# Kernel optimization log

Hardware: AMD Instinct MI355X
Metric: run time of the kernel (lower is better)

## Reference

```python
import jax, jax.numpy as jnp
import numpy as np

B, N, D, H, DH = 1, 192, 128, 4, 32
INNER = H * DH  # == D


def _ln(x, g, b):
    mu = x.mean(-1, keepdims=True)
    var = ((x - mu) ** 2).mean(-1, keepdims=True)
    return (x - mu) * jax.lax.rsqrt(var + 1e-5) * g + b


def _axial(x, row, lng, lnb, wq, wkv, wo, bo, wg, bg, wb):
    # x: (B, N, N, D). row=True: attend along axis 2 (rows as batch);
    # row=False: attend along axis 1 (columns as batch).
    scale = DH ** -0.5
    # edge bias from RAW x (edges are not layer-normed in the torch code)
    bias = jnp.einsum('bijd,dh->bhij', x, wb)            # (B, H, N, N)
    xn = _ln(x, lng, lnb)
    xa = xn if row else jnp.swapaxes(xn, 1, 2)           # (B, R, S, D)
    q = (xa @ wq).reshape(B, N, N, H, DH) * scale
    kv = (xa @ wkv).reshape(B, N, N, 2, H, DH)           # chunk(2): k then v
    k, v = kv[..., 0, :, :], kv[..., 1, :, :]
    # scores: (B, R, H, q, k); same bias matrix broadcast over every row/col R
    dots = jnp.einsum('brqhe,brkhe->brhqk', q, k) + bias[:, None]
    attn = jax.nn.softmax(dots, axis=-1)
    o = jnp.einsum('brhqk,brkhe->brqhe', attn, v).reshape(B, N, N, INNER)
    gates = jax.nn.sigmoid(xa @ wg + bg)                 # sigmoid gating on pre-attn x
    out = (o * gates) @ wo + bo
    return out if row else jnp.swapaxes(out, 1, 2)


def setup_inputs() -> dict:
    key = jax.random.key(0)
    ks = iter(jax.random.split(key, 32))

    def w(shape, s=0.02):
        return jax.random.normal(next(ks), shape, dtype=jnp.float32) * s

    inp = {"x": jax.random.normal(next(ks), (B, N, N, D), dtype=jnp.float32)}
    for sfx in ("o", "i"):  # outgoing (row) / ingoing (col) triangle attention
        inp[f"lng_{sfx}"] = jnp.ones((D,), jnp.float32)
        inp[f"lnb_{sfx}"] = jnp.zeros((D,), jnp.float32)
        inp[f"wq_{sfx}"] = w((D, INNER))
        inp[f"wkv_{sfx}"] = w((D, 2 * INNER))
        inp[f"wo_{sfx}"] = w((INNER, D))
        inp[f"bo_{sfx}"] = jnp.zeros((D,), jnp.float32)
        inp[f"wg_{sfx}"] = w((D, INNER))
        inp[f"bg_{sfx}"] = jnp.ones((INNER,), jnp.float32)  # gating bias init = 1
        inp[f"wb_{sfx}"] = w((D, H))
    inp["lng_f"] = jnp.ones((D,), jnp.float32)
    inp["lnb_f"] = jnp.zeros((D,), jnp.float32)
    inp["w1"] = w((D, 8 * D))      # dim -> dim*mult*2, mult=4
    inp["b1"] = jnp.zeros((8 * D,), jnp.float32)
    inp["w2"] = w((4 * D, D))
    inp["b2"] = jnp.zeros((D,), jnp.float32)
    return inp


def reference(x, lng_o, lnb_o, wq_o, wkv_o, wo_o, bo_o, wg_o, bg_o, wb_o,
              lng_i, lnb_i, wq_i, wkv_i, wo_i, bo_i, wg_i, bg_i, wb_i,
              lng_f, lnb_f, w1, b1, w2, b2):
    x = _axial(x, True, lng_o, lnb_o, wq_o, wkv_o, wo_o, bo_o, wg_o, bg_o, wb_o) + x
    x = _axial(x, False, lng_i, lnb_i, wq_i, wkv_i, wo_i, bo_i, wg_i, bg_i, wb_i) + x
    xn = _ln(x, lng_f, lnb_f)
    h = xn @ w1 + b1
    a, g = jnp.split(h, 2, axis=-1)   # GEGLU: x * gelu(gates), exact gelu
    ff = (a * jax.nn.gelu(g, approximate=False)) @ w2 + b2
    return x + ff
```

## Files before the change

kernel.cpp:

```cpp
#include <hip/hip_runtime.h>
#include <hip/hip_bf16.h>
#include <math.h>

constexpr int NSEQ = 192;
constexpr int DIM  = 128;
constexpr int NH   = 4;
constexpr int DHEAD = 32;
constexpr int MROWS = NSEQ * NSEQ;

typedef __hip_bfloat16 bf16;
typedef __attribute__((ext_vector_type(8))) short bf16x8;
typedef __attribute__((ext_vector_type(4))) float f32x4;
typedef unsigned int u32;

__device__ __forceinline__ void gload16(const void* g, void* l) {
    __builtin_amdgcn_global_load_lds(
        (const __attribute__((address_space(1))) u32*)g,
        (__attribute__((address_space(3))) u32*)l, 16, 0, 0);
}

__device__ __forceinline__ short f2bs(float f) {
    __hip_bfloat16 h = __float2bfloat16(f);
    return *(short*)&h;
}
__device__ __forceinline__ float bs2f(unsigned short s) {
    return __uint_as_float(((u32)s) << 16);
}

__global__ __launch_bounds__(256)
void convert_weights(const float* __restrict__ wq_o, const float* __restrict__ wkv_o,
                     const float* __restrict__ wg_o,
                     const float* __restrict__ wq_i, const float* __restrict__ wkv_i,
                     const float* __restrict__ wg_i,
                     const float* __restrict__ wo_o, const float* __restrict__ wo_i,
                     const float* __restrict__ w1, const float* __restrict__ b1,
                     const float* __restrict__ w2,
                     bf16* __restrict__ WQKVG_O, bf16* __restrict__ WQKVG_I,
                     bf16* __restrict__ WOT_O, bf16* __restrict__ WOT_I,
                     bf16* __restrict__ W1PT, bf16* __restrict__ W2T,
                     float* __restrict__ B1P)
{
    int idx = blockIdx.x * 256 + threadIdx.x;
    const float scale = 0.17677669529663689f;
    if (idx < 131072) {
        int s = idx >> 16, i = idx & 65535;
        int r = i >> 7, d = i & 127;
        const float* wq  = s ? wq_i  : wq_o;
        const float* wkv = s ? wkv_i : wkv_o;
        const float* wg  = s ? wg_i  : wg_o;
        float v;
        if (r < 128)      v = wq[d * 128 + r] * scale;
        else if (r < 384) v = wkv[d * 256 + (r - 128)];
        else              v = wg[d * 128 + (r - 384)];
        (s ? WQKVG_I : WQKVG_O)[i] = __float2bfloat16(v);
    } else if (idx < 163840) {
        int i = idx - 131072; int s = i >> 14; i &= 16383;
        int r = i >> 7, d = i & 127;
        (s ? WOT_I : WOT_O)[i] = __float2bfloat16((s ? wo_i : wo_o)[d * 128 + r]);
    } else if (idx < 294912) {
        int i = idx - 163840;
        int r = i >> 7, d = i & 127;
        int col = (r & 1) ? 512 + (r >> 1) : (r >> 1);
        W1PT[i] = __float2bfloat16(w1[d * 1024 + col]);
    } else if (idx < 360448) {
        int i = idx - 294912;
        int n = i >> 9, k = i & 511;
        W2T[i] = __float2bfloat16(w2[k * 128 + n]);
    } else if (idx < 361472) {
        int r = idx - 360448;
        B1P[r] = b1[(r & 1) ? 512 + (r >> 1) : (r >> 1)];
    }
}

__global__ __launch_bounds__(256)
void ln_bias_kernel(const float* __restrict__ x, const float* __restrict__ g,
                    const float* __restrict__ b, const float* __restrict__ wb,
                    bf16* __restrict__ xa, float* __restrict__ bias, int trans)
{
    int wid  = threadIdx.x >> 6;
    int lane = threadIdx.x & 63;
    int row  = blockIdx.x * 4 + wid;
    const float* xr = x + (size_t)row * DIM;
    float x0 = xr[lane], x1 = xr[lane + 64];
    float s = x0 + x1, sq = x0 * x0 + x1 * x1;
    #pragma unroll
    for (int off = 32; off > 0; off >>= 1) {
        s  += __shfl_down(s, off);
        sq += __shfl_down(sq, off);
    }
    s = __shfl(s, 0); sq = __shfl(sq, 0);
    float mu  = s * (1.0f / 128.0f);
    float var = sq * (1.0f / 128.0f) - mu * mu;
    float rs  = rsqrtf(var + 1e-5f);
    float y0 = (x0 - mu) * rs * g[lane]      + b[lane];
    float y1 = (x1 - mu) * rs * g[lane + 64] + b[lane + 64];
    int orow = row;
    if (trans) { int i = row / NSEQ, j = row % NSEQ; orow = j * NSEQ + i; }
    bf16* yr = xa + (size_t)orow * DIM;
    yr[lane]      = __float2bfloat16(y0);
    yr[lane + 64] = __float2bfloat16(y1);
    if (wb) {
        #pragma unroll
        for (int h = 0; h < NH; ++h) {
            float bh = x0 * wb[lane * NH + h] + x1 * wb[(lane + 64) * NH + h];
            #pragma unroll
            for (int off = 32; off > 0; off >>= 1) bh += __shfl_down(bh, off);
            if (lane == 0) bias[(size_t)h * MROWS + row] = bh;
        }
    }
}

enum { EPI_QKVG = 0, EPI_OUT = 1, EPI_GEGLU = 2, EPI_FF2 = 3 };

template<int EPI, int BM, int K>
__global__ __launch_bounds__(256)
void mfma_gemm(const bf16* __restrict__ A, const bf16* __restrict__ BT,
               const float* __restrict__ e_bias,
               const float* __restrict__ e_resid,
               float* __restrict__ e_outf,
               bf16* __restrict__ e_outb,
               bf16* __restrict__ e_outb2,
               int trans)
{
    constexpr int MREP = BM / 32;
    constexpr int ABYTES = BM * 256;
    constexpr int STAGEB = ABYTES + 32768;
    constexpr int EPIB = BM * 512;
    constexpr int LDSB = STAGEB > EPIB ? STAGEB : EPIB;
    __shared__ char sm[LDSB];
    char* asb = sm;
    char* bsb = sm + ABYTES;
    float* eb = (float*)sm;

    int tid = threadIdx.x;
    int l = tid & 63, w = tid >> 6;
    int wr = w >> 1, wc = w & 1;
    int m0 = blockIdx.x * BM, n0 = blockIdx.y * 128;
    int fr = l & 15, g = l >> 4;
    int srow  = tid >> 4;
    int satom = (tid & 15) ^ (srow & 7);

    f32x4 acc[MREP][4] = {};

    for (int k0 = 0; k0 < K; k0 += 128) {
        #pragma unroll
        for (int i = 0; i < BM / 16; ++i)
            gload16(A + (size_t)(m0 + i * 16 + srow) * K + k0 + satom * 8,
                    asb + i * 4096 + w * 1024);
        #pragma unroll
        for (int i = 0; i < 8; ++i)
            gload16(BT + (size_t)(n0 + i * 16 + srow) * K + k0 + satom * 8,
                    bsb + i * 4096 + w * 1024);
        __syncthreads();
        #pragma unroll
        for (int kk = 0; kk < 4; ++kk) {
            bf16x8 af[MREP], bfr[4];
            #pragma unroll
            for (int mi = 0; mi < MREP; ++mi) {
                int r = wr * (BM / 2) + mi * 16 + fr;
                af[mi] = *(const bf16x8*)(asb + r * 256 + ((kk * 64 + g * 16) ^ ((r & 7) << 4)));
            }
            #pragma unroll
            for (int ni = 0; ni < 4; ++ni) {
                int r = wc * 64 + ni * 16 + fr;
                bfr[ni] = *(const bf16x8*)(bsb + r * 256 + ((kk * 64 + g * 16) ^ ((r & 7) << 4)));
            }
            #pragma unroll
            for (int mi = 0; mi < MREP; ++mi)
                #pragma unroll
                for (int ni = 0; ni < 4; ++ni)
                    acc[mi][ni] = __builtin_amdgcn_mfma_f32_16x16x32_bf16(
                        af[mi], bfr[ni], acc[mi][ni], 0, 0, 0);
        }
        __syncthreads();
    }

    #pragma unroll
    for (int mi = 0; mi < MREP; ++mi)
        #pragma unroll
        for (int ni = 0; ni < 4; ++ni)
            #pragma unroll
            for (int j = 0; j < 4; ++j) {
                int rl = wr * (BM / 2) + mi * 16 + g * 4 + j;
                int cl = wc * 64 + ni * 16 + fr;
                int a  = ((cl >> 2) + rl) & 31;
                eb[rl * 128 + (a << 2) + (cl & 3)] = acc[mi][ni][j];
            }
    __syncthreads();

    #pragma unroll
    for (int p = 0; p < BM / 32; ++p) {
        int c = tid + p * 256;
        int row = c >> 3;
        int ch = c & 7;
        int grow = m0 + row;
        int gc0 = ch * 16;
        float v[16];
        #pragma unroll
        for (int q = 0; q < 4; ++q) {
            f32x4 t4 = *(const f32x4*)&eb[row * 128 + (((ch * 4 + q + row) & 31) << 2)];
            v[q * 4 + 0] = t4[0]; v[q * 4 + 1] = t4[1];
            v[q * 4 + 2] = t4[2]; v[q * 4 + 3] = t4[3];
        }
        if (EPI == EPI_QKVG) {
            int seg = blockIdx.y;
            short o16[16];
            if (seg < 3) {
                #pragma unroll
                for (int i = 0; i < 16; ++i) o16[i] = f2bs(v[i]);
                int h = gc0 >> 5, e0 = gc0 & 31;
                bf16* dst = e_outb + ((size_t)(seg * NH + h) * MROWS + grow) * DHEAD + e0;
                *(uint4*)dst = *(uint4*)o16;
                *(uint4*)(dst + 8) = *(uint4*)(o16 + 8);
            } else {
                #pragma unroll
                for (int i = 0; i < 16; ++i)
                    o16[i] = f2bs(1.0f / (1.0f + __expf(-(v[i] + e_bias[gc0 + i]))));
                bf16* dst = e_outb2 + (size_t)grow * DIM + gc0;
                *(uint4*)dst = *(uint4*)o16;
                *(uint4*)(dst + 8) = *(uint4*)(o16 + 8);
            }
        } else if (EPI == EPI_OUT || EPI == EPI_FF2) {
            int orow = (EPI == EPI_OUT && trans) ? ((grow % NSEQ) * NSEQ + grow / NSEQ) : grow;
            const float* rp = e_resid + (size_t)orow * DIM + gc0;
            float* op = e_outf + (size_t)orow * DIM + gc0;
            #pragma unroll
            for (int q = 0; q < 4; ++q) {
                float4 r4 = *(const float4*)(rp + q * 4);
                float4 o4;
                o4.x = v[q*4+0] + e_bias[gc0 + q*4 + 0] + r4.x;
                o4.y = v[q*4+1] + e_bias[gc0 + q*4 + 1] + r4.y;
                o4.z = v[q*4+2] + e_bias[gc0 + q*4 + 2] + r4.z;
                o4.w = v[q*4+3] + e_bias[gc0 + q*4 + 3] + r4.w;
                *(float4*)(op + q * 4) = o4;
            }
        } else {
            short o8[8];
            #pragma unroll
            for (int t = 0; t < 8; ++t) {
                float a  = v[2*t]     + e_bias[n0 + gc0 + 2*t];
                float gg = v[2*t + 1] + e_bias[n0 + gc0 + 2*t + 1];
                float y  = 1.5957691216f * (gg + 0.044715f * gg * gg * gg);
                float ge = gg / (1.0f + __expf(-y));
                o8[t] = f2bs(a * ge);
            }
            *(uint4*)(e_outb + (size_t)grow * 512 + ((n0 + gc0) >> 1)) = *(uint4*)o8;
        }
    }
}

__global__ __launch_bounds__(256)
void attn_mfma_kernel(const bf16* __restrict__ Qh, const bf16* __restrict__ Kh,
                      const bf16* __restrict__ Vh, const float* __restrict__ BIAS,
                      const bf16* __restrict__ G, bf16* __restrict__ TMP)
{
    __shared__ unsigned short vtp[32][200];
    int h = blockIdx.x / NSEQ;
    int r = blockIdx.x % NSEQ;
    int t = threadIdx.x;
    int l = t & 63;
    int w = t >> 6;

    const bf16* vbase = Vh + ((size_t)h * MROWS + (size_t)r * NSEQ) * DHEAD;
    #pragma unroll
    for (int i = 0; i < 6; ++i) {
        int q4 = t + i * 256;
        int k = q4 >> 3, e0 = (q4 & 7) * 4;
        uint2 v = *(const uint2*)(vbase + (size_t)k * DHEAD + e0);
        int kk = k & 31, sup = k >> 5;
        int col = sup * 32 + ((kk & 15) >> 2) * 8 + (kk & 3) + ((kk >> 4) << 2);
        const unsigned short* vs = (const unsigned short*)&v;
        #pragma unroll
        for (int j = 0; j < 4; ++j) vtp[e0 + j][col] = vs[j];
    }
    __syncthreads();

    int fr = l & 15, g = l >> 4;
    int q0 = w * 48;
    const bf16*  qbase = Qh + ((size_t)h * MROWS + (size_t)r * NSEQ) * DHEAD;
    const bf16*  kbase = Kh + ((size_t)h * MROWS + (size_t)r * NSEQ) * DHEAD;
    const float* bbase = BIAS + (size_t)h * MROWS;

    bf16x8 qf[3];
    #pragma unroll
    for (int i = 0; i < 3; ++i)
        qf[i] = *(const bf16x8*)(qbase + (size_t)(q0 + i * 16 + fr) * DHEAD + g * 8);

    f32x4 ot[3][2] = {};
    float m_[3] = {-1e30f, -1e30f, -1e30f};
    float s_[3] = {};

    for (int sup = 0; sup < 6; ++sup) {
        bf16x8 kf0 = *(const bf16x8*)(kbase + (size_t)(sup * 32 + fr) * DHEAD + g * 8);
        bf16x8 kf1 = *(const bf16x8*)(kbase + (size_t)(sup * 32 + 16 + fr) * DHEAD + g * 8);
        bf16x8 pb[3];
        #pragma unroll
        for (int qt = 0; qt < 3; ++qt) {
            f32x4 z = {};
            f32x4 s0 = __builtin_amdgcn_mfma_f32_16x16x32_bf16(kf0, qf[qt], z, 0, 0, 0);
            f32x4 s1 = __builtin_amdgcn_mfma_f32_16x16x32_bf16(kf1, qf[qt], z, 0, 0, 0);
            const float* bp = bbase + (size_t)(q0 + qt * 16 + fr) * NSEQ + sup * 32 + g * 4;
            float4 b0 = *(const float4*)bp;
            float4 b1 = *(const float4*)(bp + 16);
            s0[0] += b0.x; s0[1] += b0.y; s0[2] += b0.z; s0[3] += b0.w;
            s1[0] += b1.x; s1[1] += b1.y; s1[2] += b1.z; s1[3] += b1.w;
            float tmax = fmaxf(fmaxf(fmaxf(s0[0], s0[1]), fmaxf(s0[2], s0[3])),
                               fmaxf(fmaxf(s1[0], s1[1]), fmaxf(s1[2], s1[3])));
            tmax = fmaxf(tmax, __shfl_xor(tmax, 16));
            tmax = fmaxf(tmax, __shfl_xor(tmax, 32));
            if (__any(tmax > m_[qt] + 8.0f)) {
                float mn = fmaxf(m_[qt], tmax);
                float c = __expf(m_[qt] - mn);
                s_[qt] *= c; ot[qt][0] *= c; ot[qt][1] *= c;
                m_[qt] = mn;
            }
            float p[8];
            #pragma unroll
            for (int j = 0; j < 4; ++j) p[j]     = __expf(s0[j] - m_[qt]);
            #pragma unroll
            for (int j = 0; j < 4; ++j) p[4 + j] = __expf(s1[j] - m_[qt]);
            s_[qt] += ((p[0] + p[1]) + (p[2] + p[3])) + ((p[4] + p[5]) + (p[6] + p[7]));
            bf16x8 pk;
            #pragma unroll
            for (int j = 0; j < 8; ++j) pk[j] = f2bs(p[j]);
            pb[qt] = pk;
        }
        #pragma unroll
        for (int et = 0; et < 2; ++et) {
            bf16x8 vf = *(const bf16x8*)(&vtp[et * 16 + fr][sup * 32 + g * 8]);
            #pragma unroll
            for (int qt = 0; qt < 3; ++qt)
                ot[qt][et] = __builtin_amdgcn_mfma_f32_16x16x32_bf16(vf, pb[qt], ot[qt][et], 0, 0, 0);
        }
    }

    #pragma unroll
    for (int qt = 0; qt < 3; ++qt) {
        float sq = s_[qt];
        sq += __shfl_xor(sq, 16);
        sq += __shfl_xor(sq, 32);
        float inv = 1.0f / sq;
        int q = q0 + qt * 16 + fr;
        size_t row = (size_t)r * NSEQ + q;
        #pragma unroll
        for (int et = 0; et < 2; ++et) {
            int e0 = h * DHEAD + et * 16 + g * 4;
            const bf16* gp = G + row * DIM + e0;
            u32 g01 = *(const u32*)gp;
            u32 g23 = *(const u32*)(gp + 2);
            float gx0 = __uint_as_float((g01 & 0xffffu) << 16);
            float gx1 = __uint_as_float(g01 & 0xffff0000u);
            float gx2 = __uint_as_float((g23 & 0xffffu) << 16);
            float gx3 = __uint_as_float(g23 & 0xffff0000u);
            short o4[4];
            o4[0] = f2bs(ot[qt][et][0] * inv * gx0);
            o4[1] = f2bs(ot[qt][et][1] * inv * gx1);
            o4[2] = f2bs(ot[qt][et][2] * inv * gx2);
            o4[3] = f2bs(ot[qt][et][3] * inv * gx3);
            *(uint2*)(TMP + row * DIM + e0) = *(uint2*)o4;
        }
    }
}

extern "C" void kernel_launch(void* const* d_in, const int* in_sizes, int n_in,
                              void* d_out, int out_size, void* d_ws, size_t ws_size,
                              hipStream_t stream) {
    const float* x     = (const float*)d_in[0];
    const float* lng_o = (const float*)d_in[1];
    const float* lnb_o = (const float*)d_in[2];
    const float* wq_o  = (const float*)d_in[3];
    const float* wkv_o = (const float*)d_in[4];
    const float* wo_o  = (const float*)d_in[5];
    const float* bo_o  = (const float*)d_in[6];
    const float* wg_o  = (const float*)d_in[7];
    const float* bg_o  = (const float*)d_in[8];
    const float* wb_o  = (const float*)d_in[9];
    const float* lng_i = (const float*)d_in[10];
    const float* lnb_i = (const float*)d_in[11];
    const float* wq_i  = (const float*)d_in[12];
    const float* wkv_i = (const float*)d_in[13];
    const float* wo_i  = (const float*)d_in[14];
    const float* bo_i  = (const float*)d_in[15];
    const float* wg_i  = (const float*)d_in[16];
    const float* bg_i  = (const float*)d_in[17];
    const float* wb_i  = (const float*)d_in[18];
    const float* lng_f = (const float*)d_in[19];
    const float* lnb_f = (const float*)d_in[20];
    const float* w1    = (const float*)d_in[21];
    const float* b1    = (const float*)d_in[22];
    const float* w2    = (const float*)d_in[23];
    const float* b2    = (const float*)d_in[24];

    const size_t T = (size_t)MROWS * DIM;
    char* base = (char*)d_ws;
    bf16*  XA    = (bf16*)base;  base += T * 2;
    float* X     = (float*)base; base += T * 4;
    bf16*  QKVb  = (bf16*)base;  base += 3 * T * 2;
    bf16*  Gb    = (bf16*)base;  base += T * 2;
    float* BIASb = (float*)base; base += (size_t)NH * MROWS * 4;
    bf16*  TMP   = (bf16*)base;  base += T * 2;
    bf16*  WQKVG_O = (bf16*)base; base += 512 * 128 * 2;
    bf16*  WQKVG_I = (bf16*)base; base += 512 * 128 * 2;
    bf16*  WOT_O   = (bf16*)base; base += 128 * 128 * 2;
    bf16*  WOT_I   = (bf16*)base; base += 128 * 128 * 2;
    bf16*  W1PT    = (bf16*)base; base += 1024 * 128 * 2;
    bf16*  W2T     = (bf16*)base; base += 128 * 512 * 2;
    float* B1P     = (float*)base; base += 1024 * 4;
    bf16*  H2      = (bf16*)QKVb;
    bf16*  Qhp = QKVb;
    bf16*  Khp = QKVb + T;
    bf16*  Vhp = QKVb + 2 * T;

    convert_weights<<<1412, 256, 0, stream>>>(wq_o, wkv_o, wg_o, wq_i, wkv_i, wg_i,
                                              wo_o, wo_i, w1, b1, w2,
                                              WQKVG_O, WQKVG_I, WOT_O, WOT_I,
                                              W1PT, W2T, B1P);

    dim3 gQKVG(MROWS / 128, 4), gN128(MROWS / 128, 1), gW1(MROWS / 128, 8);
    dim3 gFF2(MROWS / 64, 1);

    ln_bias_kernel<<<MROWS / 4, 256, 0, stream>>>(x, lng_o, lnb_o, wb_o, XA, BIASb, 0);
    mfma_gemm<EPI_QKVG, 128, 128><<<gQKVG, 256, 0, stream>>>(XA, WQKVG_O, bg_o, nullptr, nullptr, QKVb, Gb, 0);
    attn_mfma_kernel<<<NSEQ * NH, 256, 0, stream>>>(Qhp, Khp, Vhp, BIASb, Gb, TMP);
    mfma_gemm<EPI_OUT, 128, 128><<<gN128, 256, 0, stream>>>(TMP, WOT_O, bo_o, x, X, nullptr, nullptr, 0);

    ln_bias_kernel<<<MROWS / 4, 256, 0, stream>>>(X, lng_i, lnb_i, wb_i, XA, BIASb, 1);
    mfma_gemm<EPI_QKVG, 128, 128><<<gQKVG, 256, 0, stream>>>(XA, WQKVG_I, bg_i, nullptr, nullptr, QKVb, Gb, 0);
    attn_mfma_kernel<<<NSEQ * NH, 256, 0, stream>>>(Qhp, Khp, Vhp, BIASb, Gb, TMP);
    mfma_gemm<EPI_OUT, 128, 128><<<gN128, 256, 0, stream>>>(TMP, WOT_I, bo_i, X, X, nullptr, nullptr, 1);

    ln_bias_kernel<<<MROWS / 4, 256, 0, stream>>>(X, lng_f, lnb_f, nullptr, XA, nullptr, 0);
    mfma_gemm<EPI_GEGLU, 128, 128><<<gW1, 256, 0, stream>>>(XA, W1PT, B1P, nullptr, nullptr, H2, nullptr, 0);
    mfma_gemm<EPI_FF2, 64, 512><<<gFF2, 256, 0, stream>>>(H2, W2T, b2, X, (float*)d_out, nullptr, nullptr, 0);
}
```

Baseline: 241.0 us.

## Fuse LayerNorm and edge-bias projection into the output GEMM epilogue

The output-projection GEMM epilogue now computes the next stage's LayerNorm and the per-head edge bias from the freshly computed residual sum. It writes the normalised bf16 activations directly in the layout the next stage needs, transposed where required. This removes two standalone ln_bias kernel launches and their full re-read of the fp32 activation tensor. The GEMM also moves to a 64-wide K step with half-height epilogue staging to cut LDS usage, and declares launch bounds targeting 4 blocks per CU. The cost is more synchronisation per K loop and a heavier epilogue with cross-lane reductions.

```diff
diff --git a/kernel.cpp b/kernel.cpp
--- a/kernel.cpp
+++ b/kernel.cpp
@@ -22,9 +22,6 @@
 __device__ __forceinline__ short f2bs(float f) {
     __hip_bfloat16 h = __float2bfloat16(f);
     return *(short*)&h;
-}
-__device__ __forceinline__ float bs2f(unsigned short s) {
-    return __uint_as_float(((u32)s) << 16);
 }
 
 __global__ __launch_bounds__(256)
@@ -75,7 +72,7 @@
 __global__ __launch_bounds__(256)
 void ln_bias_kernel(const float* __restrict__ x, const float* __restrict__ g,
                     const float* __restrict__ b, const float* __restrict__ wb,
-                    bf16* __restrict__ xa, float* __restrict__ bias, int trans)
+                    bf16* __restrict__ xa, float* __restrict__ bias)
 {
     int wid  = threadIdx.x >> 6;
     int lane = threadIdx.x & 63;
@@ -94,42 +91,43 @@
     float rs  = rsqrtf(var + 1e-5f);
     float y0 = (x0 - mu) * rs * g[lane]      + b[lane];
     float y1 = (x1 - mu) * rs * g[lane + 64] + b[lane + 64];
-    int orow = row;
-    if (trans) { int i = row / NSEQ, j = row % NSEQ; orow = j * NSEQ + i; }
-    bf16* yr = xa + (size_t)orow * DIM;
+    bf16* yr = xa + (size_t)row * DIM;
     yr[lane]      = __float2bfloat16(y0);
     yr[lane + 64] = __float2bfloat16(y1);
-    if (wb) {
-        #pragma unroll
-        for (int h = 0; h < NH; ++h) {
-            float bh = x0 * wb[lane * NH + h] + x1 * wb[(lane + 64) * NH + h];
-            #pragma unroll
-            for (int off = 32; off > 0; off >>= 1) bh += __shfl_down(bh, off);
-            if (lane == 0) bias[(size_t)h * MROWS + row] = bh;
-        }
+    #pragma unroll
+    for (int h = 0; h < NH; ++h) {
+        float bh = x0 * wb[lane * NH + h] + x1 * wb[(lane + 64) * NH + h];
+        #pragma unroll
+        for (int off = 32; off > 0; off >>= 1) bh += __shfl_down(bh, off);
+        if (lane == 0) bias[(size_t)h * MROWS + row] = bh;
     }
 }
 
 enum { EPI_QKVG = 0, EPI_OUT = 1, EPI_GEGLU = 2, EPI_FF2 = 3 };
 
 template<int EPI, int BM, int K>
-__global__ __launch_bounds__(256)
+__global__ __launch_bounds__(256, 4)
 void mfma_gemm(const bf16* __restrict__ A, const bf16* __restrict__ BT,
                const float* __restrict__ e_bias,
                const float* __restrict__ e_resid,
                float* __restrict__ e_outf,
                bf16* __restrict__ e_outb,
                bf16* __restrict__ e_outb2,
+               const float* __restrict__ lng,
+               const float* __restrict__ lnb,
+               const float* __restrict__ wbp,
+               float* __restrict__ biasb,
+               bf16* __restrict__ xa,
                int trans)
 {
-    constexpr int MREP = BM / 32;
-    constexpr int ABYTES = BM * 256;
-    constexpr int STAGEB = ABYTES + 32768;
-    constexpr int EPIB = BM * 512;
-    constexpr int LDSB = STAGEB > EPIB ? STAGEB : EPIB;
+    constexpr int MREP  = BM / 32;
+    constexpr int AB    = BM * 128;
+    constexpr int STAGE = AB + 16384;
+    constexpr int EPIB  = (BM / 2) * 512;
+    constexpr int LDSB  = STAGE > EPIB ? STAGE : EPIB;
     __shared__ char sm[LDSB];
     char* asb = sm;
-    char* bsb = sm + ABYTES;
+    char* bsb = sm + AB;
     float* eb = (float*)sm;
 
     int tid = threadIdx.x;
@@ -137,33 +135,33 @@
     int wr = w >> 1, wc = w & 1;
     int m0 = blockIdx.x * BM, n0 = blockIdx.y * 128;
     int fr = l & 15, g = l >> 4;
-    int srow  = tid >> 4;
-    int satom = (tid & 15) ^ (srow & 7);
+    int lr8 = l >> 3;
+    int satom = (l & 7) ^ lr8;
 
     f32x4 acc[MREP][4] = {};
 
-    for (int k0 = 0; k0 < K; k0 += 128) {
-        #pragma unroll
-        for (int i = 0; i < BM / 16; ++i)
-            gload16(A + (size_t)(m0 + i * 16 + srow) * K + k0 + satom * 8,
+    for (int k0 = 0; k0 < K; k0 += 64) {
+        #pragma unroll
+        for (int i = 0; i < BM / 32; ++i)
+            gload16(A + (size_t)(m0 + i * 32 + w * 8 + lr8) * K + k0 + satom * 8,
                     asb + i * 4096 + w * 1024);
         #pragma unroll
-        for (int i = 0; i < 8; ++i)
-            gload16(BT + (size_t)(n0 + i * 16 + srow) * K + k0 + satom * 8,
+        for (int i = 0; i < 4; ++i)
+            gload16(BT + (size_t)(n0 + i * 32 + w * 8 + lr8) * K + k0 + satom * 8,
                     bsb + i * 4096 + w * 1024);
         __syncthreads();
         #pragma unroll
-        for (int kk = 0; kk < 4; ++kk) {
+        for (int kk = 0; kk < 2; ++kk) {
             bf16x8 af[MREP], bfr[4];
             #pragma unroll
             for (int mi = 0; mi < MREP; ++mi) {
                 int r = wr * (BM / 2) + mi * 16 + fr;
-                af[mi] = *(const bf16x8*)(asb + r * 256 + ((kk * 64 + g * 16) ^ ((r & 7) << 4)));
+                af[mi] = *(const bf16x8*)(asb + r * 128 + ((kk * 64 + g * 16) ^ ((r & 7) << 4)));
             }
             #pragma unroll
             for (int ni = 0; ni < 4; ++ni) {
                 int r = wc * 64 + ni * 16 + fr;
-                bfr[ni] = *(const bf16x8*)(bsb + r * 256 + ((kk * 64 + g * 16) ^ ((r & 7) << 4)));
+                bfr[ni] = *(const bf16x8*)(bsb + r * 128 + ((kk * 64 + g * 16) ^ ((r & 7) << 4)));
             }
             #pragma unroll
             for (int mi = 0; mi < MREP; ++mi)
@@ -176,76 +174,131 @@
     }
 
     #pragma unroll
-    for (int mi = 0; mi < MREP; ++mi)
-        #pragma unroll
-        for (int ni = 0; ni < 4; ++ni)
-            #pragma unroll
-            for (int j = 0; j < 4; ++j) {
-                int rl = wr * (BM / 2) + mi * 16 + g * 4 + j;
-                int cl = wc * 64 + ni * 16 + fr;
-                int a  = ((cl >> 2) + rl) & 31;
-                eb[rl * 128 + (a << 2) + (cl & 3)] = acc[mi][ni][j];
+    for (int rr = 0; rr < 2; ++rr) {
+        if (wr == rr) {
+            #pragma unroll
+            for (int mi = 0; mi < MREP; ++mi)
+                #pragma unroll
+                for (int ni = 0; ni < 4; ++ni)
+                    #pragma unroll
+                    for (int j = 0; j < 4; ++j) {
+                        int rl = mi * 16 + g * 4 + j;
+                        int cl = wc * 64 + ni * 16 + fr;
+                        int a  = cl >> 2;
+                        int pa = (((a >> 2) + (a & 3)) & 7) | ((a & 3) << 3);
+                        eb[rl * 128 + pa * 4 + (cl & 3)] = acc[mi][ni][j];
+                    }
+        }
+        __syncthreads();
+        #pragma unroll
+        for (int p = 0; p < BM / 64; ++p) {
+            int c = tid + p * 256;
+            int row_l = c >> 3, ch = c & 7;
+            int grow = m0 + rr * (BM / 2) + row_l;
+            int gc0 = ch * 16;
+            float v[16];
+            #pragma unroll
+            for (int q = 0; q < 4; ++q) {
+                int pa = ((ch + q) & 7) + q * 8;
+                f32x4 t4 = *(const f32x4*)&eb[row_l * 128 + pa * 4];
+                v[q * 4 + 0] = t4[0]; v[q * 4 + 1] = t4[1];
+                v[q * 4 + 2] = t4[2]; v[q * 4 + 3] = t4[3];
             }
-    __syncthreads();
-
-    #pragma unroll
-    for (int p = 0; p < BM / 32; ++p) {
-        int c = tid + p * 256;
-        int row = c >> 3;
-        int ch = c & 7;
-        int grow = m0 + row;
-        int gc0 = ch * 16;
-        float v[16];
-        #pragma unroll
-        for (int q = 0; q < 4; ++q) {
-            f32x4 t4 = *(const f32x4*)&eb[row * 128 + (((ch * 4 + q + row) & 31) << 2)];
-            v[q * 4 + 0] = t4[0]; v[q * 4 + 1] = t4[1];
-            v[q * 4 + 2] = t4[2]; v[q * 4 + 3] = t4[3];
-        }
-        if (EPI == EPI_QKVG) {
-            int seg = blockIdx.y;
-            short o16[16];
-            if (seg < 3) {
-                #pragma unroll
-                for (int i = 0; i < 16; ++i) o16[i] = f2bs(v[i]);
-                int h = gc0 >> 5, e0 = gc0 & 31;
-                bf16* dst = e_outb + ((size_t)(seg * NH + h) * MROWS + grow) * DHEAD + e0;
-                *(uint4*)dst = *(uint4*)o16;
-                *(uint4*)(dst + 8) = *(uint4*)(o16 + 8);
+            if (EPI == EPI_QKVG) {
+                int seg = blockIdx.y;
+                short o16[16];
+                if (seg < 3) {
+                    #pragma unroll
+                    for (int i = 0; i < 16; ++i) o16[i] = f2bs(v[i]);
+                    int h = ch >> 1, e0 = (ch & 1) * 16;
+                    bf16* dst = e_outb + ((size_t)(seg * NH + h) * MROWS + grow) * DHEAD + e0;
+                    *(uint4*)dst = *(uint4*)o16;
+                    *(uint4*)(dst + 8) = *(uint4*)(o16 + 8);
+                } else {
+                    #pragma unroll
+                    for (int i = 0; i < 16; ++i)
+                        o16[i] = f2bs(1.0f / (1.0f + __expf(-(v[i] + e_bias[gc0 + i]))));
+                    bf16* dst = e_outb2 + (size_t)grow * DIM + gc0;
+                    *(uint4*)dst = *(uint4*)o16;
+                    *(uint4*)(dst + 8) = *(uint4*)(o16 + 8);
+                }
+            } else if (EPI == EPI_OUT) {
+                int orow  = trans ? ((grow % NSEQ) * NSEQ + grow / NSEQ) : grow;
+                int xarow = (grow % NSEQ) * NSEQ + grow / NSEQ;
+                const float* rp = e_resid + (size_t)orow * DIM + gc0;
+                float* op = e_outf + (size_t)orow * DIM + gc0;
+                #pragma unroll
+                for (int q = 0; q < 4; ++q) {
+                    float4 r4 = *(const float4*)(rp + q * 4);
+                    v[q*4+0] += e_bias[gc0 + q*4 + 0] + r4.x;
+                    v[q*4+1] += e_bias[gc0 + q*4 + 1] + r4.y;
+                    v[q*4+2] += e_bias[gc0 + q*4 + 2] + r4.z;
+                    v[q*4+3] += e_bias[gc0 + q*4 + 3] + r4.w;
+                    *(float4*)(op + q * 4) = make_float4(v[q*4+0], v[q*4+1], v[q*4+2], v[q*4+3]);
+                }
+                float s1 = 0.f, s2 = 0.f;
+                #pragma unroll
+                for (int i = 0; i < 16; ++i) { s1 += v[i]; s2 += v[i] * v[i]; }
+                #pragma unroll
+                for (int off = 1; off < 8; off <<= 1) {
+                    s1 += __shfl_xor(s1, off);
+                    s2 += __shfl_xor(s2, off);
+                }
+                float mu  = s1 * (1.0f / 128.0f);
+                float var = s2 * (1.0f / 128.0f) - mu * mu;
+                float rs  = rsqrtf(var + 1e-5f);
+                short o16[16];
+                #pragma unroll
+                for (int i = 0; i < 16; ++i)
+                    o16[i] = f2bs((v[i] - mu) * rs * lng[gc0 + i] + lnb[gc0 + i]);
+                bf16* xd = xa + (size_t)xarow * DIM + gc0;
+                *(uint4*)xd = *(uint4*)o16;
+                *(uint4*)(xd + 8) = *(uint4*)(o16 + 8);
+                if (wbp) {
+                    float bh[NH] = {};
+                    #pragma unroll
+                    for (int i = 0; i < 16; ++i) {
+                        float vv = v[i];
+                        #pragma unroll
+                        for (int h = 0; h < NH; ++h)
+                            bh[h] = fmaf(vv, wbp[(gc0 + i) * NH + h], bh[h]);
+                    }
+                    #pragma unroll
+                    for (int off = 1; off < 8; off <<= 1)
+                        #pragma unroll
+                        for (int h = 0; h < NH; ++h) bh[h] += __shfl_xor(bh[h], off);
+                    if (ch == 0)
+                        #pragma unroll
+                        for (int h = 0; h < NH; ++h)
+                            biasb[(size_t)h * MROWS + grow] = bh[h];
+                }
+            } else if (EPI == EPI_FF2) {
+                const float* rp = e_resid + (size_t)grow * DIM + gc0;
+                float* op = e_outf + (size_t)grow * DIM + gc0;
+                #pragma unroll
+                for (int q = 0; q < 4; ++q) {
+                    float4 r4 = *(const float4*)(rp + q * 4);
+                    float4 o4;
+                    o4.x = v[q*4+0] + e_bias[gc0 + q*4 + 0] + r4.x;
+                    o4.y = v[q*4+1] + e_bias[gc0 + q*4 + 1] + r4.y;
+                    o4.z = v[q*4+2] + e_bias[gc0 + q*4 + 2] + r4.z;
+                    o4.w = v[q*4+3] + e_bias[gc0 + q*4 + 3] + r4.w;
+                    *(float4*)(op + q * 4) = o4;
+                }
             } else {
-                #pragma unroll
-                for (int i = 0; i < 16; ++i)
-                    o16[i] = f2bs(1.0f / (1.0f + __expf(-(v[i] + e_bias[gc0 + i]))));
-                bf16* dst = e_outb2 + (size_t)grow * DIM + gc0;
-                *(uint4*)dst = *(uint4*)o16;
-                *(uint4*)(dst + 8) = *(uint4*)(o16 + 8);
+                short o8[8];
+                #pragma unroll
+                for (int t = 0; t < 8; ++t) {
+                    float a  = v[2*t]     + e_bias[n0 + gc0 + 2*t];
+                    float gg = v[2*t + 1] + e_bias[n0 + gc0 + 2*t + 1];
+                    float y  = 1.5957691216f * (gg + 0.044715f * gg * gg * gg);
+                    float ge = gg / (1.0f + __expf(-y));
+                    o8[t] = f2bs(a * ge);
+                }
+                *(uint4*)(e_outb + (size_t)grow * 512 + ((n0 + gc0) >> 1)) = *(uint4*)o8;
             }
-        } else if (EPI == EPI_OUT || EPI == EPI_FF2) {
-            int orow = (EPI == EPI_OUT && trans) ? ((grow % NSEQ) * NSEQ + grow / NSEQ) : grow;
-            const float* rp = e_resid + (size_t)orow * DIM + gc0;
-            float* op = e_outf + (size_t)orow * DIM + gc0;
-            #pragma unroll
-            for (int q = 0; q < 4; ++q) {
-                float4 r4 = *(const float4*)(rp + q * 4);
-                float4 o4;
-                o4.x = v[q*4+0] + e_bias[gc0 + q*4 + 0] + r4.x;
-                o4.y = v[q*4+1] + e_bias[gc0 + q*4 + 1] + r4.y;
-                o4.z = v[q*4+2] + e_bias[gc0 + q*4 + 2] + r4.z;
-                o4.w = v[q*4+3] + e_bias[gc0 + q*4 + 3] + r4.w;
-                *(float4*)(op + q * 4) = o4;
-            }
-        } else {
-            short o8[8];
-            #pragma unroll
-            for (int t = 0; t < 8; ++t) {
-                float a  = v[2*t]     + e_bias[n0 + gc0 + 2*t];
-                float gg = v[2*t + 1] + e_bias[n0 + gc0 + 2*t + 1];
-                float y  = 1.5957691216f * (gg + 0.044715f * gg * gg * gg);
-                float ge = gg / (1.0f + __expf(-y));
-                o8[t] = f2bs(a * ge);
-            }
-            *(uint4*)(e_outb + (size_t)grow * 512 + ((n0 + gc0) >> 1)) = *(uint4*)o8;
-        }
+        }
+        __syncthreads();
     }
 }
 
@@ -416,20 +469,30 @@
                                               WQKVG_O, WQKVG_I, WOT_O, WOT_I,
                                               W1PT, W2T, B1P);
 
-    dim3 gQKVG(MROWS / 128, 4), gN128(MROWS / 128, 1), gW1(MROWS / 128, 8);
+    dim3 gQKVG(MROWS / 128, 4), gOUT(MROWS / 128, 1), gW1(MROWS / 128, 8);
     dim3 gFF2(MROWS / 64, 1);
 
-    ln_bias_kernel<<<MROWS / 4, 256, 0, stream>>>(x, lng_o, lnb_o, wb_o, XA, BIASb, 0);
-    mfma_gemm<EPI_QKVG, 128, 128><<<gQKVG, 256, 0, stream>>>(XA, WQKVG_O, bg_o, nullptr, nullptr, QKVb, Gb, 0);
+    ln_bias_kernel<<<MROWS / 4, 256, 0, stream>>>(x, lng_o, lnb_o, wb_o, XA, BIASb);
+    mfma_gemm<EPI_QKVG, 128, 128><<<gQKVG, 256, 0, stream>>>(
+        XA, WQKVG_O, bg_o, nullptr, nullptr, QKVb, Gb,
+        nullptr, nullptr, nullptr, nullptr, nullptr, 0);
     attn_mfma_kernel<<<NSEQ * NH, 256, 0, stream>>>(Qhp, Khp, Vhp, BIASb, Gb, TMP);
-    mfma_gemm<EPI_OUT, 128, 128><<<gN128, 256, 0, stream>>>(TMP, WOT_O, bo_o, x, X, nullptr, nullptr, 0);
-
-    ln_bias_kernel<<<MROWS / 4, 256, 0, stream>>>(X, lng_i, lnb_i, wb_i, XA, BIASb, 1);
-    mfma_gemm<EPI_QKVG, 128, 128><<<gQKVG, 256, 0, stream>>>(XA, WQKVG_I, bg_i, nullptr, nullptr, QKVb, Gb, 0);
+    mfma_gemm<EPI_OUT, 128, 128><<<gOUT, 256, 0, stream>>>(
+        TMP, WOT_O, bo_o, x, X, nullptr, nullptr,
+        lng_i, lnb_i, wb_i, BIASb, XA, 0);
+
+    mfma_gemm<EPI_QKVG, 128, 128><<<gQKVG, 256, 0, stream>>>(
+        XA, WQKVG_I, bg_i, nullptr, nullptr, QKVb, Gb,
+        nullptr, nullptr, nullptr, nullptr, nullptr, 0);
     attn_mfma_kernel<<<NSEQ * NH, 256, 0, stream>>>(Qhp, Khp, Vhp, BIASb, Gb, TMP);
-    mfma_gemm<EPI_OUT, 128, 128><<<gN128, 256, 0, stream>>>(TMP, WOT_I, bo_i, X, X, nullptr, nullptr, 1);
-
-    ln_bias_kernel<<<MROWS / 4, 256, 0, stream>>>(X, lng_f, lnb_f, nullptr, XA, nullptr, 0);
-    mfma_gemm<EPI_GEGLU, 128, 128><<<gW1, 256, 0, stream>>>(XA, W1PT, B1P, nullptr, nullptr, H2, nullptr, 0);
-    mfma_gemm<EPI_FF2, 64, 512><<<gFF2, 256, 0, stream>>>(H2, W2T, b2, X, (float*)d_out, nullptr, nullptr, 0);
-}
+    mfma_gemm<EPI_OUT, 128, 128><<<gOUT, 256, 0, stream>>>(
+        TMP, WOT_I, bo_i, X, X, nullptr, nullptr,
+        lng_f, lnb_f, nullptr, nullptr, XA, 1);
+
+    mfma_gemm<EPI_GEGLU, 128, 128><<<gW1, 256, 0, stream>>>(
+        XA, W1PT, B1P, nullptr, nullptr, H2, nullptr,
+        nullptr, nullptr, nullptr, nullptr, nullptr, 0);
+    mfma_gemm<EPI_FF2, 64, 512><<<gFF2, 256, 0, stream>>>(
+        H2, W2T, b2, X, (float*)d_out, nullptr, nullptr,
+        nullptr, nullptr, nullptr, nullptr, nullptr, 0);
+}
```

Result: faster. 231.2 us (-4.1%).
